# Kernel tuning notes

Hardware: AMD Instinct MI355X
Metric: run time of the kernel (lower is better)

## Reference

```python
import jax, jax.numpy as jnp
import numpy as np

N, M, D, G, E = 1024, 1024, 1024, 16, 64  # rois, ref rois, feat_dim, groups, emb_dim
DG = D // G  # 64 per-group dim


def _make_boxes(k, n):
    k1, k2 = jax.random.split(k)
    xy = jax.random.uniform(k1, (n, 2), dtype=jnp.float32) * 500.0
    wh = jax.random.uniform(k2, (n, 2), dtype=jnp.float32) * 100.0 + 1.0
    return jnp.concatenate([xy, xy + wh], axis=1)  # [n,4] xmin,ymin,xmax,ymax


def setup_inputs() -> dict:
    key = jax.random.key(0)
    ks = jax.random.split(key, 10)
    s = 0.02
    return {
        "roi_feat": jax.random.normal(ks[0], (N, D), dtype=jnp.float32),
        "ref_feat": jax.random.normal(ks[1], (M, D), dtype=jnp.float32),
        "rois1": _make_boxes(ks[2], N),
        "rois2": _make_boxes(ks[3], M),
        "Wq": jax.random.normal(ks[4], (D, D), dtype=jnp.float32) * s,
        "bq": jnp.zeros((D,), jnp.float32),
        "Wk": jax.random.normal(ks[5], (D, D), dtype=jnp.float32) * s,
        "bk": jnp.zeros((D,), jnp.float32),
        "Wg": jax.random.normal(ks[6], (G, E), dtype=jnp.float32) * s,
        "bg": jnp.zeros((G,), jnp.float32),
        "Wv": jax.random.normal(ks[7], (G, DG, D), dtype=jnp.float32) * s,
        "bv": jnp.zeros((D,), jnp.float32),
    }


def _position_matrix(bbox, ref_bbox):
    # bbox [N,4], ref_bbox [M,4] -> [N,M,4]
    def parts(b):
        xmin, ymin, xmax, ymax = b[:, 0], b[:, 1], b[:, 2], b[:, 3]
        w = xmax - xmin + 1.0
        h = ymax - ymin + 1.0
        cx = 0.5 * (xmin + xmax)
        cy = 0.5 * (ymin + ymax)
        return w, h, cx, cy

    w, h, cx, cy = parts(bbox)            # [N]
    wr, hr, cxr, cyr = parts(ref_bbox)    # [M]
    dx = jnp.log(jnp.abs((cx[:, None] - cxr[None, :]) / w[:, None]) + 1e-3)
    dy = jnp.log(jnp.abs((cy[:, None] - cyr[None, :]) / h[:, None]) + 1e-3)
    dw = jnp.log(w[:, None] / wr[None, :])
    dh = jnp.log(h[:, None] / hr[None, :])
    return jnp.stack([dx, dy, dw, dh], axis=2)  # [N,M,4]


def _position_embedding(pos_mat, feat_dim=64, wave_length=1000.0):
    fr = jnp.arange(feat_dim // 8, dtype=jnp.float32)            # [8]
    dim_mat = jnp.power(wave_length, (8.0 / feat_dim) * fr)      # [8]
    div = pos_mat[..., None] * 100.0 / dim_mat                   # [N,M,4,8]
    emb = jnp.concatenate([jnp.sin(div), jnp.cos(div)], axis=3)  # [N,M,4,16]
    return emb.reshape(pos_mat.shape[0], pos_mat.shape[1], -1)   # [N,M,64]


def reference(roi_feat, ref_feat, rois1, rois2, Wq, bq, Wk, bk, Wg, bg, Wv, bv):
    # position embedding: [N,M,E]
    pos_emb = _position_embedding(_position_matrix(rois1, rois2), feat_dim=E)
    # Wgs 1x1 conv (E -> G) + relu -> aff_weight [N,G,M]
    aff_weight = jax.nn.relu(jnp.einsum("nme,ge->ngm", pos_emb, Wg) + bg[None, :, None])
    # grouped q/k projections
    q = (roi_feat @ Wq + bq).reshape(N, G, DG)   # [N,G,dg]
    k = (ref_feat @ Wk + bk).reshape(M, G, DG)   # [M,G,dg]
    aff = jnp.einsum("ngd,mgd->ngm", q, k) * (1.0 / np.sqrt(DG))
    weighted = jnp.log(aff_weight + 1e-6) + aff  # [N,G,M]
    sm = jax.nn.softmax(weighted, axis=2)
    out_t = jnp.einsum("ngm,md->ngd", sm, ref_feat)          # [N,G,D]
    out = jnp.einsum("ngd,god->ngo", out_t, Wv).reshape(N, D) + bv  # grouped 1x1 conv
    return out
```

## Files before the change

### kernel.cpp

```cpp
#include <hip/hip_runtime.h>
#include <hip/hip_fp16.h>
#include <cstddef>
#include <cstdint>

#define N_ 1024
#define M_ 1024
#define D_ 1024
#define G_ 16
#define DG_ 64

typedef __bf16 bf16x8 __attribute__((ext_vector_type(8)));
typedef _Float16 f16x8 __attribute__((ext_vector_type(8)));
typedef float f32x4 __attribute__((ext_vector_type(4)));

typedef __attribute__((address_space(1))) const void* gas_ptr;
typedef __attribute__((address_space(3))) void* las_ptr;

__device__ __forceinline__ void gl_lds16(const void* g, void* l) {
    __builtin_amdgcn_global_load_lds((gas_ptr)g, (las_ptr)l, 16, 0, 0);
}

__device__ __forceinline__ size_t qkf_idx(int g, int rb, int ks, int lane) {
    return ((((size_t)(g * 64 + rb)) * 2 + ks) * 64 + lane) * 8;
}
__device__ __forceinline__ size_t vf_idx(int g, int ot, int mc, int lane) {
    return ((((size_t)(g * 4 + ot)) * 32 + mc) * 64 + lane) * 8;
}
__device__ __forceinline__ size_t awt_idx(int g, int mb, int n, int quad) {
    return (((size_t)(mb * 1024 + n)) * 16 + g) * 16 + quad * 4;
}

__global__ __launch_bounds__(256)
void prep_pos(const float* __restrict__ roi, const float* __restrict__ ref,
              const float* __restrict__ Wq, const float* __restrict__ Wk,
              const float* __restrict__ Wv,
              __bf16* __restrict__ roiB, __bf16* __restrict__ refB,
              __bf16* __restrict__ WqT, __bf16* __restrict__ WkT,
              __bf16* __restrict__ WvR,
              const float* __restrict__ rois1, const float* __restrict__ rois2,
              const float* __restrict__ Wg, const float* __restrict__ bg,
              __half* __restrict__ AWt)
{
    __shared__ float tls[64][65];
    const int b = blockIdx.x;
    const int tid = threadIdx.x;
    const int w = tid >> 6, lane = tid & 63;
    const int quad = lane >> 4, l15 = lane & 15;

    if (b < 1024) {
        const int n = b;
        const float xmin = rois1[n * 4 + 0], ymin = rois1[n * 4 + 1];
        const float xmax = rois1[n * 4 + 2], ymax = rois1[n * 4 + 3];
        const float wn  = xmax - xmin + 1.f, hn  = ymax - ymin + 1.f;
        const float cxn = 0.5f * (xmin + xmax), cyn = 0.5f * (ymin + ymax);
        const float rwn = 1.0f / wn, rhn = 1.0f / hn;
        const float lwn = __logf(wn), lhn = __logf(hn);

        f16x8 wgf[2];
        #pragma unroll
        for (int ks = 0; ks < 2; ++ks) {
            const float* p = &Wg[l15 * 64 + ks * 32 + quad * 8];
            float4 a = *(const float4*)p;
            float4 bb = *(const float4*)(p + 4);
            wgf[ks][0] = (_Float16)a.x; wgf[ks][1] = (_Float16)a.y;
            wgf[ks][2] = (_Float16)a.z; wgf[ks][3] = (_Float16)a.w;
            wgf[ks][4] = (_Float16)bb.x; wgf[ks][5] = (_Float16)bb.y;
            wgf[ks][6] = (_Float16)bb.z; wgf[ks][7] = (_Float16)bb.w;
        }
        const float bgv = bg[l15];

        const float fr8[8] = {100.0f, 42.16965f, 17.782794f, 7.4989421f,
                              3.1622777f, 1.3335214f, 0.56234133f, 0.23713737f};
        const float phase = (quad & 1) ? 1.5707963267948966f : 0.f;

        for (int mq = 0; mq < 4; ++mq) {
            const int m0w = mq * 256 + w * 64;
            #pragma unroll
            for (int ti = 0; ti < 4; ++ti) {
                const int mt0 = m0w + ti * 16;
                const int m = mt0 + l15;
                float4 r2 = *(const float4*)&rois2[m * 4];
                const float wr  = r2.z - r2.x + 1.f, hr  = r2.w - r2.y + 1.f;
                const float cxr = 0.5f * (r2.x + r2.z), cyr = 0.5f * (r2.y + r2.w);

                const float f0 = __logf(fabsf((cxn - cxr) * rwn) + 0.001f);
                const float f1 = __logf(fabsf((cyn - cyr) * rhn) + 0.001f);
                const float f2 = lwn - __logf(wr);
                const float f3 = lhn - __logf(hr);
                const float fa = (quad & 2) ? f1 : f0;
                const float fb = (quad & 2) ? f3 : f2;

                f32x4 acc = {};
                #pragma unroll
                for (int ks = 0; ks < 2; ++ks) {
                    const float feat = ks ? fb : fa;
                    f16x8 ef;
                    #pragma unroll
                    for (int j = 0; j < 8; ++j)
                        ef[j] = (_Float16)__sinf(fmaf(feat, fr8[j], phase));
                    acc = __builtin_amdgcn_mfma_f32_16x16x32_f16(ef, wgf[ks], acc, 0, 0, 0);
                }

                __half p[4];
                #pragma unroll
                for (int r = 0; r < 4; ++r)
                    p[r] = __float2half(fmaxf(acc[r] + bgv, 0.f) + 1e-6f);
                *(uint2*)&AWt[awt_idx(l15, mt0 >> 4, n, quad)] = *(const uint2*)p;
            }
        }
        return;
    }

    if (b < 1216) {
        const int cbk = b - 1024;
        const int mat = cbk >> 6;
        const float* S = (mat == 0) ? roi : (mat == 1) ? ref : Wv;
        __bf16* Dt = (mat == 0) ? roiB : (mat == 1) ? refB : WvR;
        const int base = (cbk & 63) * 16384;
        #pragma unroll
        for (int i = 0; i < 16; ++i) {
            const int e = base + i * 1024 + tid * 4;
            float4 v = *(const float4*)&S[e];
            __bf16 p[4] = {(__bf16)v.x, (__bf16)v.y, (__bf16)v.z, (__bf16)v.w};
            *(uint2*)&Dt[e] = *(const uint2*)p;
        }
        return;
    }

    const int tb = b - 1216;
    const int mat = tb >> 8;
    const float* S = mat ? Wk : Wq;
    __bf16* Dt = mat ? WkT : WqT;
    const int tile = tb & 255;
    const int k0 = (tile >> 4) * 64, j0 = (tile & 15) * 64;

    #pragma unroll
    for (int rr = 0; rr < 4; ++rr) {
        const int row = (tid >> 4) * 4 + rr;
        const int col = (tid & 15) * 4;
        float4 v = *(const float4*)&S[(size_t)(k0 + row) * 1024 + j0 + col];
        tls[row][col + 0] = v.x; tls[row][col + 1] = v.y;
        tls[row][col + 2] = v.z; tls[row][col + 3] = v.w;
    }
    __syncthreads();
    #pragma unroll
    for (int rr = 0; rr < 4; ++rr) {
        const int j = (tid >> 4) * 4 + rr;
        const int kc = (tid & 15) * 4;
        __bf16 p[4] = {(__bf16)tls[kc + 0][j], (__bf16)tls[kc + 1][j],
                       (__bf16)tls[kc + 2][j], (__bf16)tls[kc + 3][j]};
        *(uint2*)&Dt[(size_t)(j0 + j) * 1024 + k0 + kc] = *(const uint2*)p;
    }
}

__global__ __launch_bounds__(256)
void gemm_qkv2(const __bf16* __restrict__ roiB, const __bf16* __restrict__ refB,
               const __bf16* __restrict__ WqT, const __bf16* __restrict__ WkT,
               const __bf16* __restrict__ WvR,
               const float* __restrict__ bq, const float* __restrict__ bk,
               __bf16* __restrict__ Qf, __bf16* __restrict__ Kf,
               __bf16* __restrict__ Vf)
{
    __shared__ __align__(16) char smem[49152];
    const int b = blockIdx.x;
    const int tid = threadIdx.x;
    const int w = tid >> 6, lane = tid & 63;
    const int quad = lane >> 4, l15 = lane & 15;

    const int z = b >> 7, t6 = b & 127;
    const __bf16* A = (z == 0) ? roiB : refB;
    const __bf16* Bm = (z == 0) ? WqT : (z == 1) ? WkT : WvR;
    const int i0 = (t6 >> 4) * 128, j0 = (t6 & 15) * 64;
    const int iw = (w & 1) * 64, jw = (w >> 1) * 32;

    const int gcolc = (((lane & 7) ^ (lane >> 3)) << 4);
    const char* asrc[4];
    const char* bsrc[2];
    #pragma unroll
    for (int it = 0; it < 4; ++it) {
        const int row = (w * 4 + it) * 8 + (lane >> 3);
        asrc[it] = (const char*)A + (size_t)(i0 + row) * 2048 + gcolc;
    }
    #pragma unroll
    for (int it = 0; it < 2; ++it) {
        const int row = (w * 2 + it) * 8 + (lane >> 3);
        bsrc[it] = (const char*)Bm + (size_t)(j0 + row) * 2048 + gcolc;
    }

    const int swm = (l15 & 7) << 4;
    const int off0 = l15 * 128 + ((quad * 16) ^ swm);
    const int off1 = l15 * 128 + ((64 + quad * 16) ^ swm);

    f32x4 acc[4][2] = {};

    #define STAGE(c, kb)                                                        \
        do {                                                                    \
            _Pragma("unroll")                                                   \
            for (int it = 0; it < 4; ++it)                                      \
                gl_lds16(asrc[it] + (kb),                                       \
                         smem + (c) * 16384 + (w * 4 + it) * 1024);             \
            _Pragma("unroll")                                                   \
            for (int it = 0; it < 2; ++it)                                      \
                gl_lds16(bsrc[it] + (kb),                                       \
                         smem + 32768 + (c) * 8192 + (w * 2 + it) * 1024);      \
        } while (0)

    STAGE(0, 0);
    int cur = 0;
    for (int t = 0; t < 16; ++t) {
        if (t < 15) {
            STAGE(cur ^ 1, (t + 1) * 128);
            asm volatile("s_waitcnt vmcnt(6)" ::: "memory");
        } else {
            asm volatile("s_waitcnt vmcnt(0)" ::: "memory");
        }
        __builtin_amdgcn_s_barrier();

        const char* Ab = smem + cur * 16384;
        const char* Bb = smem + 32768 + cur * 8192;
        #pragma unroll
        for (int ks = 0; ks < 2; ++ks) {
            const int offk = ks ? off1 : off0;
            bf16x8 af[4], bfr[2];
            #pragma unroll
            for (int t4 = 0; t4 < 4; ++t4)
                af[t4] = *(const bf16x8*)(Ab + (iw + t4 * 16) * 128 + offk);
            #pragma unroll
            for (int t4 = 0; t4 < 2; ++t4)
                bfr[t4] = *(const bf16x8*)(Bb + (jw + t4 * 16) * 128 + offk);
            #pragma unroll
            for (int ti = 0; ti < 4; ++ti)
                #pragma unroll
                for (int tj = 0; tj < 2; ++tj)
                    acc[ti][tj] = __builtin_amdgcn_mfma_f32_16x16x32_bf16(
                        af[ti], bfr[tj], acc[ti][tj], 0, 0, 0);
        }
        asm volatile("s_waitcnt lgkmcnt(0)" ::: "memory");
        __builtin_amdgcn_s_barrier();
        cur ^= 1;
    }
    #undef STAGE

    if (z < 2) {
        const float* bias = (z == 0) ? bq : bk;
        __bf16* dst = (z == 0) ? Qf : Kf;
        const float scale = (z == 0) ? 0.125f : 1.0f;
        #pragma unroll
        for (int ti = 0; ti < 4; ++ti) {
            const int rb = (i0 + iw + ti * 16) >> 4;
            #pragma unroll
            for (int tj = 0; tj < 2; ++tj) {
                const int go = j0 + jw + tj * 16 + l15;
                const int g = go >> 6, ks = (go >> 5) & 1;
                const int lanef = ((go >> 3) & 3) * 16;
                const int jf = go & 7;
                const float bb = bias[go];
                __bf16* base = dst + qkf_idx(g, rb, ks, 0) + jf;
                #pragma unroll
                for (int r = 0; r < 4; ++r)
                    base[(size_t)(lanef + quad * 4 + r) * 8] =
                        (__bf16)((acc[ti][tj][r] + bb) * scale);
            }
        }
    } else {
        #pragma unroll
        for (int ti = 0; ti < 4; ++ti) {
            const int mbase = i0 + iw + ti * 16 + quad * 4;
            const int mc = mbase >> 5, quadv = (mbase >> 3) & 3, jb = mbase & 7;
            #pragma unroll
            for (int tj = 0; tj < 2; ++tj) {
                const int go = j0 + jw + tj * 16 + l15;
                const int g = go >> 6, ot = (go >> 4) & 3, o15 = go & 15;
                __bf16 p[4];
                #pragma unroll
                for (int r = 0; r < 4; ++r) p[r] = (__bf16)acc[ti][tj][r];
                *(uint2*)&Vf[vf_idx(g, ot, mc, quadv * 16 + o15) + jb] =
                    *(const uint2*)p;
            }
        }
    }
}

__global__ __launch_bounds__(256)
void attn_mfma(const __bf16* __restrict__ Qf, const __bf16* __restrict__ Kf,
               const __bf16* __restrict__ Vf, const __half* __restrict__ AWt,
               const float* __restrict__ bv, float* __restrict__ out)
{
    __shared__ __align__(16) char smem[17664];

    const int tid = threadIdx.x;
    const int w = tid >> 6, lane = tid & 63;
    const int quad = lane >> 4, l15 = lane & 15;
    const int nb = blockIdx.x, n0 = nb * 16, g = blockIdx.y;

    __bf16(*Psw)[72] = (__bf16(*)[72])(smem + w * 2304);
    float(*accb)[64][17] = (float(*)[64][17])smem;
    float(*lsb)[16] = (float(*)[16])(smem + 17408);

    bf16x8 qf[2];
    qf[0] = *(const bf16x8*)&Qf[qkf_idx(g, nb, 0, lane)];
    qf[1] = *(const bf16x8*)&Qf[qkf_idx(g, nb, 1, lane)];

    f32x4 acc[4] = {};
    float llocal = 0.f;

    #pragma unroll
    for (int t64 = 0; t64 < 4; ++t64) {
        const int mt = w * 4 + t64;

        f32x4 s[4];
        #pragma unroll
        for (int t = 0; t < 4; ++t) {
            bf16x8 ka0 = *(const bf16x8*)&Kf[qkf_idx(g, mt * 4 + t, 0, lane)];
            bf16x8 ka1 = *(const bf16x8*)&Kf[qkf_idx(g, mt * 4 + t, 1, lane)];
            f32x4 z = {};
            __builtin_amdgcn_s_setprio(1);
            z = __builtin_amdgcn_mfma_f32_16x16x32_bf16(ka0, qf[0], z, 0, 0, 0);
            s[t] = __builtin_amdgcn_mfma_f32_16x16x32_bf16(ka1, qf[1], z, 0, 0, 0);
            __builtin_amdgcn_s_setprio(0);
        }

        #pragma unroll
        for (int t = 0; t < 4; ++t) {
            uint2 au = *(const uint2*)&AWt[awt_idx(g, mt * 4 + t, n0 + l15, quad)];
            const __half* a4 = (const __half*)&au;
            __bf16 pk[4];
            #pragma unroll
            for (int r = 0; r < 4; ++r) {
                const float p = __half2float(a4[r]) * __expf(s[t][r]);
                llocal += p;
                pk[r] = (__bf16)p;
            }
            *(uint2*)&Psw[l15][t * 16 + quad * 4] = *(const uint2*)pk;
        }

        #pragma unroll
        for (int mcl = 0; mcl < 2; ++mcl) {
            bf16x8 pbf = *(const bf16x8*)&Psw[l15][mcl * 32 + quad * 8];
            __builtin_amdgcn_s_setprio(1);
            #pragma unroll
            for (int ot = 0; ot < 4; ++ot) {
                bf16x8 va = *(const bf16x8*)&Vf[vf_idx(g, ot, mt * 2 + mcl, lane)];
                acc[ot] = __builtin_amdgcn_mfma_f32_16x16x32_bf16(va, pbf, acc[ot], 0, 0, 0);
            }
            __builtin_amdgcn_s_setprio(0);
        }
    }

    llocal += __shfl_xor(llocal, 16, 64);
    llocal += __shfl_xor(llocal, 32, 64);

    __syncthreads();

    #pragma unroll
    for (int ot = 0; ot < 4; ++ot)
        #pragma unroll
        for (int r = 0; r < 4; ++r)
            accb[w][ot * 16 + quad * 4 + r][l15] = acc[ot][r];
    if (quad == 0) lsb[w][l15] = llocal;
    __syncthreads();

    const float lt = lsb[0][l15] + lsb[1][l15] + lsb[2][l15] + lsb[3][l15];
    const float inv = 1.f / lt;
    #pragma unroll
    for (int r = 0; r < 4; ++r) {
        const int o = w * 16 + quad * 4 + r;
        const int ogl = g * 64 + o;
        const float v = accb[0][o][l15] + accb[1][o][l15] +
                        accb[2][o][l15] + accb[3][o][l15];
        out[(size_t)(n0 + l15) * D_ + ogl] = v * inv + bv[ogl];
    }
}

extern "C" void kernel_launch(void* const* d_in, const int* in_sizes, int n_in,
                              void* d_out, int out_size, void* d_ws, size_t ws_size,
                              hipStream_t stream) {
    const float* roi_feat = (const float*)d_in[0];
    const float* ref_feat = (const float*)d_in[1];
    const float* rois1    = (const float*)d_in[2];
    const float* rois2    = (const float*)d_in[3];
    const float* Wq       = (const float*)d_in[4];
    const float* bq       = (const float*)d_in[5];
    const float* Wk       = (const float*)d_in[6];
    const float* bk       = (const float*)d_in[7];
    const float* Wg       = (const float*)d_in[8];
    const float* bg       = (const float*)d_in[9];
    const float* Wv       = (const float*)d_in[10];
    const float* bv       = (const float*)d_in[11];
    float* out = (float*)d_out;

    char* ws = (char*)d_ws;
    __bf16* Qf   = (__bf16*)(ws + 0);
    __bf16* Kf   = (__bf16*)(ws + (2u << 20));
    __bf16* Vf   = (__bf16*)(ws + (4u << 20));
    __half* AWt  = (__half*)(ws + (6u << 20));
    __bf16* roiB = (__bf16*)(ws + (40u << 20));
    __bf16* refB = (__bf16*)(ws + (42u << 20));
    __bf16* WqT  = (__bf16*)(ws + (44u << 20));
    __bf16* WkT  = (__bf16*)(ws + (46u << 20));
    __bf16* WvR  = (__bf16*)(ws + (48u << 20));

    dim3 blk(256);
    prep_pos<<<dim3(1728), blk, 0, stream>>>(roi_feat, ref_feat, Wq, Wk, Wv,
                                             roiB, refB, WqT, WkT, WvR,
                                             rois1, rois2, Wg, bg, AWt);
    gemm_qkv2<<<dim3(384), blk, 0, stream>>>(roiB, refB, WqT, WkT, WvR,
                                             bq, bk, Qf, Kf, Vf);
    attn_mfma<<<dim3(64, 16), blk, 0, stream>>>(Qf, Kf, Vf, AWt, bv, out);
}
```

Baseline: 138.2 us.

## Retile affinity-weight layout per block and batch-prefetch K/V/AW loads in attention

Changes the AWt storage layout so that each (group, 16-row n-block, m-block) slab is contiguous, making the attention kernel's per-block reads of position weights dense instead of strided across the whole n dimension. Inside the attention kernel, all K, V and AW loads for one m-chunk are issued up front into registers before the MFMAs, to overlap memory latency. The outer loop is no longer unrolled and launch bounds request two blocks per SM. Costs are more live registers per iteration and a possible occupancy limit.

Result: no change. 140.0 us (+1.3%).

```diff
diff --git a/kernel.cpp b/kernel.cpp
--- a/kernel.cpp
+++ b/kernel.cpp
@@ -26,8 +26,9 @@
 __device__ __forceinline__ size_t vf_idx(int g, int ot, int mc, int lane) {
     return ((((size_t)(g * 4 + ot)) * 32 + mc) * 64 + lane) * 8;
 }
-__device__ __forceinline__ size_t awt_idx(int g, int mb, int n, int quad) {
-    return (((size_t)(mb * 1024 + n)) * 16 + g) * 16 + quad * 4;
+__device__ __forceinline__ size_t awt_idx(int g, int nb, int mb, int n16, int q4) {
+    size_t slab = ((size_t)(g * 64 + nb) * 64 + mb);
+    return slab * 256 + n16 * 16 + q4 * 4;
 }
 
 __global__ __launch_bounds__(256)
@@ -49,6 +50,7 @@
 
     if (b < 1024) {
         const int n = b;
+        const int nbw = n >> 4, n16 = n & 15;
         const float xmin = rois1[n * 4 + 0], ymin = rois1[n * 4 + 1];
         const float xmax = rois1[n * 4 + 2], ymax = rois1[n * 4 + 3];
         const float wn  = xmax - xmin + 1.f, hn  = ymax - ymin + 1.f;
@@ -105,7 +107,7 @@
                 #pragma unroll
                 for (int r = 0; r < 4; ++r)
                     p[r] = __float2half(fmaxf(acc[r] + bgv, 0.f) + 1e-6f);
-                *(uint2*)&AWt[awt_idx(l15, mt0 >> 4, n, quad)] = *(const uint2*)p;
+                *(uint2*)&AWt[awt_idx(l15, nbw, mt0 >> 4, n16, quad)] = *(const uint2*)p;
             }
         }
         return;
@@ -281,10 +283,10 @@
     }
 }
 
-__global__ __launch_bounds__(256)
-void attn_mfma(const __bf16* __restrict__ Qf, const __bf16* __restrict__ Kf,
-               const __bf16* __restrict__ Vf, const __half* __restrict__ AWt,
-               const float* __restrict__ bv, float* __restrict__ out)
+__global__ __launch_bounds__(256, 2)
+void attn_mfma5(const __bf16* __restrict__ Qf, const __bf16* __restrict__ Kf,
+                const __bf16* __restrict__ Vf, const __half* __restrict__ AWt,
+                const float* __restrict__ bv, float* __restrict__ out)
 {
     __shared__ __align__(16) char smem[17664];
 
@@ -304,26 +306,40 @@
     f32x4 acc[4] = {};
     float llocal = 0.f;
 
-    #pragma unroll
+    #pragma unroll 1
     for (int t64 = 0; t64 < 4; ++t64) {
         const int mt = w * 4 + t64;
 
+        bf16x8 ka0[4], ka1[4];
+        uint2 au[4];
+        bf16x8 va[8];
+        #pragma unroll
+        for (int t = 0; t < 4; ++t) {
+            ka0[t] = *(const bf16x8*)&Kf[qkf_idx(g, mt * 4 + t, 0, lane)];
+            ka1[t] = *(const bf16x8*)&Kf[qkf_idx(g, mt * 4 + t, 1, lane)];
+        }
+        #pragma unroll
+        for (int t = 0; t < 4; ++t)
+            au[t] = *(const uint2*)&AWt[awt_idx(g, nb, mt * 4 + t, l15, quad)];
+        #pragma unroll
+        for (int mcl = 0; mcl < 2; ++mcl)
+            #pragma unroll
+            for (int ot = 0; ot < 4; ++ot)
+                va[mcl * 4 + ot] = *(const bf16x8*)&Vf[vf_idx(g, ot, mt * 2 + mcl, lane)];
+
         f32x4 s[4];
         #pragma unroll
         for (int t = 0; t < 4; ++t) {
-            bf16x8 ka0 = *(const bf16x8*)&Kf[qkf_idx(g, mt * 4 + t, 0, lane)];
-            bf16x8 ka1 = *(const bf16x8*)&Kf[qkf_idx(g, mt * 4 + t, 1, lane)];
             f32x4 z = {};
             __builtin_amdgcn_s_setprio(1);
-            z = __builtin_amdgcn_mfma_f32_16x16x32_bf16(ka0, qf[0], z, 0, 0, 0);
-            s[t] = __builtin_amdgcn_mfma_f32_16x16x32_bf16(ka1, qf[1], z, 0, 0, 0);
+            z = __builtin_amdgcn_mfma_f32_16x16x32_bf16(ka0[t], qf[0], z, 0, 0, 0);
+            s[t] = __builtin_amdgcn_mfma_f32_16x16x32_bf16(ka1[t], qf[1], z, 0, 0, 0);
             __builtin_amdgcn_s_setprio(0);
         }
 
         #pragma unroll
         for (int t = 0; t < 4; ++t) {
-            uint2 au = *(const uint2*)&AWt[awt_idx(g, mt * 4 + t, n0 + l15, quad)];
-            const __half* a4 = (const __half*)&au;
+            const __half* a4 = (const __half*)&au[t];
             __bf16 pk[4];
             #pragma unroll
             for (int r = 0; r < 4; ++r) {
@@ -339,10 +355,9 @@
             bf16x8 pbf = *(const bf16x8*)&Psw[l15][mcl * 32 + quad * 8];
             __builtin_amdgcn_s_setprio(1);
             #pragma unroll
-            for (int ot = 0; ot < 4; ++ot) {
-                bf16x8 va = *(const bf16x8*)&Vf[vf_idx(g, ot, mt * 2 + mcl, lane)];
-                acc[ot] = __builtin_amdgcn_mfma_f32_16x16x32_bf16(va, pbf, acc[ot], 0, 0, 0);
-            }
+            for (int ot = 0; ot < 4; ++ot)
+                acc[ot] = __builtin_amdgcn_mfma_f32_16x16x32_bf16(
+                    va[mcl * 4 + ot], pbf, acc[ot], 0, 0, 0);
             __builtin_amdgcn_s_setprio(0);
         }
     }
@@ -406,5 +421,5 @@
                                              rois1, rois2, Wg, bg, AWt);
     gemm_qkv2<<<dim3(384), blk, 0, stream>>>(roiB, refB, WqT, WkT, WvR,
                                              bq, bk, Qf, Kf, Vf);
-    attn_mfma<<<dim3(64, 16), blk, 0, stream>>>(Qf, Kf, Vf, AWt, bv, out);
-}
+    attn_mfma5<<<dim3(64, 16), blk, 0, stream>>>(Qf, Kf, Vf, AWt, bv, out);
+}
```
